# Performance work log

Hardware: AMD Instinct MI355X
Metric: run time of the kernel (lower is better)

## Reference

```python
import jax, jax.numpy as jnp
import numpy as np

N_GRAPHS = 256
RATIO = 0.5


def setup_inputs() -> dict:
    key = jax.random.key(0)
    k0, k1, k2, k3, k4 = jax.random.split(key, 5)
    N, E, D = 100000, 1600000, 64
    x = jax.random.normal(k0, (N, D), dtype=jnp.float32)
    edge_index = jax.random.randint(k1, (2, E), 0, N, dtype=jnp.int32)
    batch = jnp.sort(jax.random.randint(k2, (N,), 0, N_GRAPHS, dtype=jnp.int32))
    # GraphConv(in_channels=64, out_channels=1) parameters
    w_rel = jax.random.normal(k3, (D,), dtype=jnp.float32) * 0.1
    b_rel = jnp.zeros((), dtype=jnp.float32)
    w_root = jax.random.normal(k4, (D,), dtype=jnp.float32) * 0.1
    return {"x": x, "edge_index": edge_index, "batch": batch,
            "w_rel": w_rel, "b_rel": b_rel, "w_root": w_root}


def reference(x, edge_index, batch, w_rel, b_rel, w_root):
    N = x.shape[0]
    src, dst = edge_index[0], edge_index[1]
    # GraphConv score: lin_rel(sum_{j in N(i)} x_j) + lin_root(x_i)
    agg = jax.ops.segment_sum(x[src], dst, num_segments=N)        # [N, D]
    score = jnp.tanh(agg @ w_rel + b_rel + x @ w_root)            # [N], SAGPool tanh
    # per-graph topk: keep k_g = ceil(ratio * n_g) highest-score nodes
    sizes = jax.ops.segment_sum(jnp.ones(N, jnp.int32), batch,
                                num_segments=N_GRAPHS)            # [G]
    k = jnp.ceil(RATIO * sizes.astype(jnp.float32)).astype(jnp.int32)
    starts = jnp.concatenate([jnp.zeros(1, jnp.int32),
                              jnp.cumsum(sizes)[:-1].astype(jnp.int32)])
    order = jnp.lexsort((-score, batch))                          # graph-major, score desc
    rank = jnp.arange(N, dtype=jnp.int32) - starts[batch[order]]  # rank within graph
    keep_sorted = rank < k[batch[order]]
    keep = jnp.zeros(N, dtype=bool).at[order].set(keep_sorted)
    # kept nodes are scaled by their tanh score; dropped nodes contribute 0
    w = jnp.where(keep, score, jnp.zeros_like(score))             # [N]
    num = jax.ops.segment_sum(x * w[:, None], batch, num_segments=N_GRAPHS)
    cnt = jax.ops.segment_sum(keep.astype(x.dtype), batch, num_segments=N_GRAPHS)
    return num / jnp.maximum(cnt, 1.0)[:, None]                   # global_mean_pool
```

## Files before the change

kernel.cpp:

```cpp
#include <hip/hip_runtime.h>

#define NGRAPHS 256
#define CHUNK 4096
#define BINR 256
#define CAPB 6144
#define MAXB 512
#define NMAX 2048

__global__ __launch_bounds__(512) void k1_fused(
    const float* __restrict__ x,
    const int*   __restrict__ batch,
    const int*   __restrict__ ei,
    const float* __restrict__ w_rel,
    const float* __restrict__ w_root,
    float* __restrict__ p, float* __restrict__ r,
    int* __restrict__ starts, int* __restrict__ ends,
    int* __restrict__ C,
    int N, int E, int NBLKE, int NBINS, int vecE)
{
    __shared__ int hist[MAXB];
    int tid = threadIdx.x;

    if ((int)blockIdx.x < NBLKE) {
        for (int b = tid; b < NBINS; b += 512) hist[b] = 0;
        __syncthreads();
        int beg = blockIdx.x * CHUNK;
        int end = min(beg + CHUNK, E);
        if (vecE) {
            const int4* d4 = (const int4*)(ei + E);
            for (int i = (beg >> 2) + tid; i < (end >> 2); i += 512) {
                int4 d = d4[i];
                atomicAdd(&hist[d.x >> 8], 1);
                atomicAdd(&hist[d.y >> 8], 1);
                atomicAdd(&hist[d.z >> 8], 1);
                atomicAdd(&hist[d.w >> 8], 1);
            }
        } else {
            for (int i = beg + tid; i < end; i += 512)
                atomicAdd(&hist[ei[E + i] >> 8], 1);
        }
        __syncthreads();
        for (int b = tid; b < NBINS; b += 512)
            C[(size_t)blockIdx.x * NBINS + b] = hist[b];
        return;
    }

    int row = ((int)blockIdx.x - NBLKE) * 32 + (tid >> 4);
    int fq  = tid & 15;
    if (row >= N) return;
    if (fq == 0) {
        int b = batch[row];
        if (row == 0) {
            for (int g = 0; g < b; ++g) { starts[g] = 0; ends[g] = 0; }
            starts[b] = 0;
        } else {
            int bp = batch[row - 1];
            if (bp != b) {
                ends[bp] = row;
                for (int g = bp + 1; g < b; ++g) { starts[g] = row; ends[g] = row; }
                starts[b] = row;
            }
        }
        if (row == N - 1) {
            ends[b] = N;
            for (int g = b + 1; g < NGRAPHS; ++g) { starts[g] = N; ends[g] = N; }
        }
    }
    float4 v  = *(const float4*)(x + (size_t)row * 64 + fq * 4);
    float4 wr = ((const float4*)w_rel)[fq];
    float4 wo = ((const float4*)w_root)[fq];
    float a = v.x * wr.x + v.y * wr.y + v.z * wr.z + v.w * wr.w;
    float c = v.x * wo.x + v.y * wo.y + v.z * wo.z + v.w * wo.w;
    a += __shfl_down(a, 8); c += __shfl_down(c, 8);
    a += __shfl_down(a, 4); c += __shfl_down(c, 4);
    a += __shfl_down(a, 2); c += __shfl_down(c, 2);
    a += __shfl_down(a, 1); c += __shfl_down(c, 1);
    if (fq == 0) { p[row] = a; r[row] = c; }
}

__global__ __launch_bounds__(512) void kA2_scan(
    int* __restrict__ C, int* __restrict__ cursor, int NBLK, int NBINS)
{
    __shared__ int sh[512];
    int b = blockIdx.x;
    int t = threadIdx.x;
    int c = (t < NBLK) ? C[(size_t)t * NBINS + b] : 0;
    sh[t] = c;
    __syncthreads();
    #pragma unroll
    for (int off = 1; off < 512; off <<= 1) {
        int v = (t >= off) ? sh[t - off] : 0;
        __syncthreads();
        sh[t] += v;
        __syncthreads();
    }
    if (t < NBLK) C[(size_t)t * NBINS + b] = b * CAPB + (sh[t] - c);
    if (t == 511) cursor[b] = sh[t];
}

__global__ __launch_bounds__(512) void kA3_scatter(
    const int* __restrict__ ei,
    const int* __restrict__ C,
    unsigned* __restrict__ bucket,
    int E, int NBINS, int vecE)
{
    __shared__ int cur[MAXB];
    int tid = threadIdx.x;
    for (int b = tid; b < NBINS; b += 512)
        cur[b] = C[(size_t)blockIdx.x * NBINS + b];
    __syncthreads();
    int beg = blockIdx.x * CHUNK;
    int end = min(beg + CHUNK, E);
    if (vecE) {
        const int4* s4 = (const int4*)ei;
        const int4* d4 = (const int4*)(ei + E);
        for (int i = (beg >> 2) + tid; i < (end >> 2); i += 512) {
            int4 d = d4[i];
            int4 s = s4[i];
            int b0 = d.x >> 8, p0 = atomicAdd(&cur[b0], 1);
            if (p0 < (b0 + 1) * CAPB) bucket[p0] = ((unsigned)s.x << 8) | (unsigned)(d.x & 255);
            int b1 = d.y >> 8, p1 = atomicAdd(&cur[b1], 1);
            if (p1 < (b1 + 1) * CAPB) bucket[p1] = ((unsigned)s.y << 8) | (unsigned)(d.y & 255);
            int b2 = d.z >> 8, p2 = atomicAdd(&cur[b2], 1);
            if (p2 < (b2 + 1) * CAPB) bucket[p2] = ((unsigned)s.z << 8) | (unsigned)(d.z & 255);
            int b3 = d.w >> 8, p3 = atomicAdd(&cur[b3], 1);
            if (p3 < (b3 + 1) * CAPB) bucket[p3] = ((unsigned)s.w << 8) | (unsigned)(d.w & 255);
        }
    } else {
        for (int i = beg + tid; i < end; i += 512) {
            int d = ei[E + i];
            int s = ei[i];
            int b = d >> 8;
            int pos = atomicAdd(&cur[b], 1);
            if (pos < (b + 1) * CAPB)
                bucket[pos] = ((unsigned)s << 8) | (unsigned)(d & 255);
        }
    }
}

__global__ __launch_bounds__(512) void kB_score(
    const unsigned* __restrict__ bucket,
    const int* __restrict__ cursor,
    const float* __restrict__ p,
    const float* __restrict__ r,
    const float* __restrict__ brel,
    float* __restrict__ score, int N)
{
    __shared__ float acc[BINR];
    int tid = threadIdx.x;
    int b   = blockIdx.x;
    if (tid < BINR) acc[tid] = 0.0f;
    __syncthreads();
    int lo  = b * CAPB;
    int cnt = min(cursor[b], CAPB);
    const uint4* bk4 = (const uint4*)(bucket + lo);
    int quart = cnt >> 2;
    for (int e = tid; e < quart; e += 512) {
        uint4 u = bk4[e];
        float v0 = p[u.x >> 8], v1 = p[u.y >> 8];
        float v2 = p[u.z >> 8], v3 = p[u.w >> 8];
        atomicAdd(&acc[u.x & 255u], v0);
        atomicAdd(&acc[u.y & 255u], v1);
        atomicAdd(&acc[u.z & 255u], v2);
        atomicAdd(&acc[u.w & 255u], v3);
    }
    int tail = cnt & 3;
    if (tid < tail) {
        unsigned u = bucket[lo + (quart << 2) + tid];
        atomicAdd(&acc[u & 255u], p[u >> 8]);
    }
    __syncthreads();
    int node = b * BINR + tid;
    if (tid < BINR && node < N)
        score[node] = tanhf(acc[tid] + brel[0] + r[node]);
}

__global__ __launch_bounds__(256) void kZ_zero(float* __restrict__ a, int N)
{
    int i = blockIdx.x * 256 + threadIdx.x;
    if (i < N) a[i] = 0.0f;
}
__global__ __launch_bounds__(256) void k2_scatter(
    const int* __restrict__ ei, const float* __restrict__ p,
    float* aggdot, int E)
{
    int i = blockIdx.x * 256 + threadIdx.x;
    if (i < E) unsafeAtomicAdd(&aggdot[ei[E + i]], p[ei[i]]);
}
__global__ __launch_bounds__(256) void kS_score(
    const float* __restrict__ aggdot, const float* __restrict__ r,
    const float* __restrict__ brel, float* __restrict__ score, int N)
{
    int i = blockIdx.x * 256 + threadIdx.x;
    if (i < N) score[i] = tanhf(aggdot[i] + brel[0] + r[i]);
}

__global__ __launch_bounds__(512) void k4_pool(
    const float* __restrict__ x,
    const float* __restrict__ score,
    const int* __restrict__ starts,
    const int* __restrict__ ends,
    float* __restrict__ out)
{
    __shared__ __align__(16) float sc[NMAX];
    __shared__ int   kidx[NMAX / 2 + 64];
    __shared__ float kw[NMAX / 2 + 64];
    __shared__ float accs[8][64][4];
    __shared__ int   pctr;

    int g   = blockIdx.x;
    int tid = threadIdx.x;
    int start = starts[g];
    int n     = ends[g] - start;
    if (n > NMAX) n = NMAX;
    int k = (n + 1) >> 1;
    if (tid == 0) pctr = 0;

    for (int i = tid; i < n; i += 512) sc[i] = score[start + i];
    __syncthreads();

    int n4 = n & ~3;
    for (int i = tid; i < n; i += 512) {
        float si = sc[i];
        int rank = 0;
        int j = 0;
        for (; j < n4; j += 4) {
            float4 s4 = *(const float4*)&sc[j];
            rank += (s4.x > si) || (s4.x == si && (j + 0) < i);
            rank += (s4.y > si) || (s4.y == si && (j + 1) < i);
            rank += (s4.z > si) || (s4.z == si && (j + 2) < i);
            rank += (s4.w > si) || (s4.w == si && (j + 3) < i);
        }
        for (; j < n; ++j) {
            float sj = sc[j];
            rank += (sj > si) || (sj == si && j < i);
        }
        if (rank < k) {
            int pos = atomicAdd(&pctr, 1);
            kidx[pos] = i;
            kw[pos]   = si;
        }
    }
    __syncthreads();
    int k32 = (k + 31) & ~31;
    for (int e = k + tid; e < k32; e += 512) { kidx[e] = 0; kw[e] = 0.0f; }
    __syncthreads();

    int wg   = tid >> 6;
    int lane = tid & 63;
    int rgrp = lane >> 4;
    int fq   = lane & 15;
    float a0 = 0.0f, a1 = 0.0f, a2 = 0.0f, a3 = 0.0f;
    #pragma unroll 2
    for (int e = wg * 4 + rgrp; e < k32; e += 32) {
        float wv = kw[e];
        int row  = start + kidx[e];
        const float4 v = *(const float4*)(x + (size_t)row * 64 + fq * 4);
        a0 += v.x * wv; a1 += v.y * wv; a2 += v.z * wv; a3 += v.w * wv;
    }
    accs[wg][lane][0] = a0; accs[wg][lane][1] = a1;
    accs[wg][lane][2] = a2; accs[wg][lane][3] = a3;
    __syncthreads();
    if (tid < 64) {
        int f = tid;
        float sum = 0.0f;
        #pragma unroll
        for (int gg = 0; gg < 8; ++gg)
            #pragma unroll
            for (int rg = 0; rg < 4; ++rg)
                sum += accs[gg][rg * 16 + (f >> 2)][f & 3];
        out[(size_t)g * 64 + f] = sum / fmaxf((float)k, 1.0f);
    }
}

extern "C" void kernel_launch(void* const* d_in, const int* in_sizes, int n_in,
                              void* d_out, int out_size, void* d_ws, size_t ws_size,
                              hipStream_t stream) {
    const float* x      = (const float*)d_in[0];
    const int*   ei     = (const int*)  d_in[1];
    const int*   batch  = (const int*)  d_in[2];
    const float* w_rel  = (const float*)d_in[3];
    const float* b_rel  = (const float*)d_in[4];
    const float* w_root = (const float*)d_in[5];
    float* out = (float*)d_out;

    int N = in_sizes[2];
    int E = in_sizes[1] / 2;
    int NBLKE = (E + CHUNK - 1) / CHUNK;
    int NBINS = (N + BINR - 1) / BINR;
    int vecE  = ((E & 3) == 0);

    float* p      = (float*)d_ws;
    float* r      = p + (size_t)N;
    float* score  = r + (size_t)N;
    int*   starts = (int*)(score + (size_t)N);
    int*   ends   = starts + NGRAPHS;
    int*   cursor = ends + NGRAPHS;
    int*   C      = cursor + MAXB;
    unsigned* bucket = (unsigned*)(C + (size_t)NBLKE * NBINS);
    size_t need = ((size_t)3 * N + 2 * NGRAPHS + MAXB
                   + (size_t)NBLKE * NBINS + (size_t)NBINS * CAPB) * 4;

    bool binned = (need <= ws_size) && (NBLKE <= 512) && (NBINS <= MAXB)
                  && (N < (1 << 24));

    int dotblks = (N + 31) / 32;
    if (binned) {
        k1_fused<<<NBLKE + dotblks, 512, 0, stream>>>(x, batch, ei, w_rel, w_root,
                                                      p, r, starts, ends, C,
                                                      N, E, NBLKE, NBINS, vecE);
        kA2_scan<<<NBINS, 512, 0, stream>>>(C, cursor, NBLKE, NBINS);
        kA3_scatter<<<NBLKE, 512, 0, stream>>>(ei, C, bucket, E, NBINS, vecE);
        kB_score<<<NBINS, 512, 0, stream>>>(bucket, cursor, p, r, b_rel, score, N);
    } else {
        float* aggdot = (float*)C;
        k1_fused<<<dotblks, 512, 0, stream>>>(x, batch, ei, w_rel, w_root,
                                              p, r, starts, ends, C, N, E, 0,
                                              NBINS, vecE);
        kZ_zero<<<(N + 255) / 256, 256, 0, stream>>>(aggdot, N);
        k2_scatter<<<(E + 255) / 256, 256, 0, stream>>>(ei, p, aggdot, E);
        kS_score<<<(N + 255) / 256, 256, 0, stream>>>(aggdot, r, b_rel, score, N);
    }
    k4_pool<<<NGRAPHS, 512, 0, stream>>>(x, score, starts, ends, out);
}
```

Before: 134.3 us.

## Fuse bucket score reduction into pool kernel and pre-gather source dots in scatter

The scatter kernel now gathers p[src] itself and writes split value (float) and local-destination (byte) bucket arrays. The separate kB_score kernel is removed, and each graph's pool block reduces the bins overlapping its node range into shared memory, then applies tanh. This removes one launch and the score round trip through global memory. In exchange, bins that straddle graph boundaries are read by two blocks, and the reduction runs on only 256 blocks, so it has less parallelism than the 391-bin kernel it replaces.

New measurement: 148.9 us. +10.9%, slower.

```diff
diff --git a/kernel.cpp b/kernel.cpp
--- a/kernel.cpp
+++ b/kernel.cpp
@@ -100,8 +100,10 @@
 
 __global__ __launch_bounds__(512) void kA3_scatter(
     const int* __restrict__ ei,
+    const float* __restrict__ p,
     const int* __restrict__ C,
-    unsigned* __restrict__ bucket,
+    float* __restrict__ bucket_v,
+    unsigned char* __restrict__ bucket_d,
     int E, int NBINS, int vecE)
 {
     __shared__ int cur[MAXB];
@@ -117,62 +119,29 @@
         for (int i = (beg >> 2) + tid; i < (end >> 2); i += 512) {
             int4 d = d4[i];
             int4 s = s4[i];
+            float v0 = p[s.x], v1 = p[s.y], v2 = p[s.z], v3 = p[s.w];
             int b0 = d.x >> 8, p0 = atomicAdd(&cur[b0], 1);
-            if (p0 < (b0 + 1) * CAPB) bucket[p0] = ((unsigned)s.x << 8) | (unsigned)(d.x & 255);
+            if (p0 < (b0 + 1) * CAPB) { bucket_v[p0] = v0; bucket_d[p0] = (unsigned char)(d.x & 255); }
             int b1 = d.y >> 8, p1 = atomicAdd(&cur[b1], 1);
-            if (p1 < (b1 + 1) * CAPB) bucket[p1] = ((unsigned)s.y << 8) | (unsigned)(d.y & 255);
+            if (p1 < (b1 + 1) * CAPB) { bucket_v[p1] = v1; bucket_d[p1] = (unsigned char)(d.y & 255); }
             int b2 = d.z >> 8, p2 = atomicAdd(&cur[b2], 1);
-            if (p2 < (b2 + 1) * CAPB) bucket[p2] = ((unsigned)s.z << 8) | (unsigned)(d.z & 255);
+            if (p2 < (b2 + 1) * CAPB) { bucket_v[p2] = v2; bucket_d[p2] = (unsigned char)(d.z & 255); }
             int b3 = d.w >> 8, p3 = atomicAdd(&cur[b3], 1);
-            if (p3 < (b3 + 1) * CAPB) bucket[p3] = ((unsigned)s.w << 8) | (unsigned)(d.w & 255);
+            if (p3 < (b3 + 1) * CAPB) { bucket_v[p3] = v3; bucket_d[p3] = (unsigned char)(d.w & 255); }
         }
     } else {
         for (int i = beg + tid; i < end; i += 512) {
             int d = ei[E + i];
             int s = ei[i];
+            float v = p[s];
             int b = d >> 8;
             int pos = atomicAdd(&cur[b], 1);
-            if (pos < (b + 1) * CAPB)
-                bucket[pos] = ((unsigned)s << 8) | (unsigned)(d & 255);
-        }
-    }
-}
-
-__global__ __launch_bounds__(512) void kB_score(
-    const unsigned* __restrict__ bucket,
-    const int* __restrict__ cursor,
-    const float* __restrict__ p,
-    const float* __restrict__ r,
-    const float* __restrict__ brel,
-    float* __restrict__ score, int N)
-{
-    __shared__ float acc[BINR];
-    int tid = threadIdx.x;
-    int b   = blockIdx.x;
-    if (tid < BINR) acc[tid] = 0.0f;
-    __syncthreads();
-    int lo  = b * CAPB;
-    int cnt = min(cursor[b], CAPB);
-    const uint4* bk4 = (const uint4*)(bucket + lo);
-    int quart = cnt >> 2;
-    for (int e = tid; e < quart; e += 512) {
-        uint4 u = bk4[e];
-        float v0 = p[u.x >> 8], v1 = p[u.y >> 8];
-        float v2 = p[u.z >> 8], v3 = p[u.w >> 8];
-        atomicAdd(&acc[u.x & 255u], v0);
-        atomicAdd(&acc[u.y & 255u], v1);
-        atomicAdd(&acc[u.z & 255u], v2);
-        atomicAdd(&acc[u.w & 255u], v3);
-    }
-    int tail = cnt & 3;
-    if (tid < tail) {
-        unsigned u = bucket[lo + (quart << 2) + tid];
-        atomicAdd(&acc[u & 255u], p[u >> 8]);
-    }
-    __syncthreads();
-    int node = b * BINR + tid;
-    if (tid < BINR && node < N)
-        score[node] = tanhf(acc[tid] + brel[0] + r[node]);
+            if (pos < (b + 1) * CAPB) {
+                bucket_v[pos] = v;
+                bucket_d[pos] = (unsigned char)(d & 255);
+            }
+        }
+    }
 }
 
 __global__ __launch_bounds__(256) void kZ_zero(float* __restrict__ a, int N)
@@ -197,9 +166,14 @@
 
 __global__ __launch_bounds__(512) void k4_pool(
     const float* __restrict__ x,
-    const float* __restrict__ score,
+    const float* __restrict__ r,
+    const float* __restrict__ brel,
     const int* __restrict__ starts,
     const int* __restrict__ ends,
+    const int* __restrict__ cursor,
+    const float* __restrict__ bucket_v,
+    const unsigned char* __restrict__ bucket_d,
+    const float* __restrict__ score,
     float* __restrict__ out)
 {
     __shared__ __align__(16) float sc[NMAX];
@@ -216,7 +190,46 @@
     int k = (n + 1) >> 1;
     if (tid == 0) pctr = 0;
 
-    for (int i = tid; i < n; i += 512) sc[i] = score[start + i];
+    if (bucket_v) {
+        for (int i = tid; i < n; i += 512) sc[i] = 0.0f;
+        __syncthreads();
+        if (n > 0) {
+            int b0 = start >> 8;
+            int b1 = (start + n - 1) >> 8;
+            for (int b = b0; b <= b1; ++b) {
+                int lo   = b * CAPB;
+                int cnt  = min(cursor[b], CAPB);
+                int base = b * BINR - start;
+                const float4* v4 = (const float4*)(bucket_v + lo);
+                const uchar4* d4 = (const uchar4*)(bucket_d + lo);
+                int quart = cnt >> 2;
+                for (int e = tid; e < quart; e += 512) {
+                    uchar4 dd = d4[e];
+                    float4 vv = v4[e];
+                    int i0 = base + dd.x;
+                    int i1 = base + dd.y;
+                    int i2 = base + dd.z;
+                    int i3 = base + dd.w;
+                    if ((unsigned)i0 < (unsigned)n) atomicAdd(&sc[i0], vv.x);
+                    if ((unsigned)i1 < (unsigned)n) atomicAdd(&sc[i1], vv.y);
+                    if ((unsigned)i2 < (unsigned)n) atomicAdd(&sc[i2], vv.z);
+                    if ((unsigned)i3 < (unsigned)n) atomicAdd(&sc[i3], vv.w);
+                }
+                int tail = cnt & 3;
+                if (tid < tail) {
+                    int e  = (quart << 2) + tid;
+                    int i0 = base + bucket_d[lo + e];
+                    if ((unsigned)i0 < (unsigned)n) atomicAdd(&sc[i0], bucket_v[lo + e]);
+                }
+            }
+        }
+        __syncthreads();
+        float bias = brel[0];
+        for (int i = tid; i < n; i += 512)
+            sc[i] = tanhf(sc[i] + bias + r[start + i]);
+    } else {
+        for (int i = tid; i < n; i += 512) sc[i] = score[start + i];
+    }
     __syncthreads();
 
     int n4 = n & ~3;
@@ -297,9 +310,11 @@
     int*   ends   = starts + NGRAPHS;
     int*   cursor = ends + NGRAPHS;
     int*   C      = cursor + MAXB;
-    unsigned* bucket = (unsigned*)(C + (size_t)NBLKE * NBINS);
+    float* bucket_v = (float*)(C + (size_t)NBLKE * NBINS);
+    unsigned char* bucket_d = (unsigned char*)(bucket_v + (size_t)NBINS * CAPB);
     size_t need = ((size_t)3 * N + 2 * NGRAPHS + MAXB
-                   + (size_t)NBLKE * NBINS + (size_t)NBINS * CAPB) * 4;
+                   + (size_t)NBLKE * NBINS + (size_t)NBINS * CAPB) * 4
+                  + (size_t)NBINS * CAPB;
 
     bool binned = (need <= ws_size) && (NBLKE <= 512) && (NBINS <= MAXB)
                   && (N < (1 << 24));
@@ -310,8 +325,10 @@
                                                       p, r, starts, ends, C,
                                                       N, E, NBLKE, NBINS, vecE);
         kA2_scan<<<NBINS, 512, 0, stream>>>(C, cursor, NBLKE, NBINS);
-        kA3_scatter<<<NBLKE, 512, 0, stream>>>(ei, C, bucket, E, NBINS, vecE);
-        kB_score<<<NBINS, 512, 0, stream>>>(bucket, cursor, p, r, b_rel, score, N);
+        kA3_scatter<<<NBLKE, 512, 0, stream>>>(ei, p, C, bucket_v, bucket_d,
+                                               E, NBINS, vecE);
+        k4_pool<<<NGRAPHS, 512, 0, stream>>>(x, r, b_rel, starts, ends, cursor,
+                                             bucket_v, bucket_d, nullptr, out);
     } else {
         float* aggdot = (float*)C;
         k1_fused<<<dotblks, 512, 0, stream>>>(x, batch, ei, w_rel, w_root,
@@ -320,6 +337,7 @@
         kZ_zero<<<(N + 255) / 256, 256, 0, stream>>>(aggdot, N);
         k2_scatter<<<(E + 255) / 256, 256, 0, stream>>>(ei, p, aggdot, E);
         kS_score<<<(N + 255) / 256, 256, 0, stream>>>(aggdot, r, b_rel, score, N);
-    }
-    k4_pool<<<NGRAPHS, 512, 0, stream>>>(x, score, starts, ends, out);
-}
+        k4_pool<<<NGRAPHS, 512, 0, stream>>>(x, r, b_rel, starts, ends, cursor,
+                                             nullptr, nullptr, score, out);
+    }
+}
```
